# Optimization experiments

Measured on AMD Instinct MI355X. Metric: run time of the kernel, lower is better.

## Reference

```python
import jax, jax.numpy as jnp
import numpy as np

O, P, G, N, H, D = 3, 128, 64, 20000, 512, 128
TEMPERATURE = 0.1
EPS = 1e-12


def setup_inputs() -> dict:
    key = jax.random.key(0)
    k0, k1, k2, k3 = jax.random.split(key, 4)
    emb = jax.random.normal(k0, (O, N, H), dtype=jnp.float32)
    idx = jax.random.randint(k1, (O, P, G), 0, N)
    W1 = jax.random.normal(k2, (O, H, H), dtype=jnp.float32) * 0.02
    b1 = jnp.zeros((O, H), dtype=jnp.float32)
    W2 = jax.random.normal(k3, (O, H, D), dtype=jnp.float32) * 0.02
    b2 = jnp.zeros((O, D), dtype=jnp.float32)
    return {"emb": emb, "W1": W1, "b1": b1, "W2": W2, "b2": b2, "idx": idx}


def reference(emb, W1, b1, W2, b2, idx):
    # Per-omics pathway prototypes: gather gene rows then mean-pool.  [O,P,H]
    protos = jax.vmap(lambda e, i: jnp.mean(e[i], axis=1))(emb, idx)
    # Per-omics projection head: Linear -> ReLU -> (Dropout=identity in eval) -> Linear
    h = jax.nn.relu(jnp.einsum('oph,ohk->opk', protos, W1) + b1[:, None, :])
    z = jnp.einsum('opk,okd->opd', h, W2) + b2[:, None, :]          # [O,P,D]
    # Original loops p outer, ntype inner -> order (pathway, omics)
    z = jnp.transpose(z, (1, 0, 2)).reshape(P * O, D)                # [M,D], M=P*O
    z = z / (jnp.linalg.norm(z, axis=-1, keepdims=True) + EPS)       # l2 normalize
    y = jnp.repeat(jnp.arange(P), O)                                 # pathway labels [M]

    sim = (z @ z.T) / TEMPERATURE                                    # [M,M]
    M = sim.shape[0]
    eye = jnp.eye(M, dtype=bool)
    sim = jnp.where(eye, -jnp.inf, sim)
    pos_mask = (y[None, :] == y[:, None]) & ~eye
    exp_sim = jnp.exp(sim)                                           # exp(-inf)=0 on diagonal
    denom = exp_sim.sum(axis=1) + EPS
    pos_sum = jnp.sum(exp_sim * pos_mask.astype(exp_sim.dtype), axis=1) + EPS
    # every anchor has O-1 positives here, so all anchors are valid
    loss = -jnp.log(pos_sum / denom)
    return loss.mean()
```

## Files before the change

### kernel.cpp

```cpp
#include <hip/hip_runtime.h>
#include <math.h>

#define O_ 3
#define P_ 128
#define G_ 64
#define N_ 20000
#define H_ 512
#define D_ 128
#define M_ (O_*P_)
#define R_ 4

static constexpr float TEMP_INV = 10.0f;
static constexpr float EPS_ = 1e-12f;

__global__ __launch_bounds__(512) void k_proto_gemm1(const float* __restrict__ emb,
                                                     const int* __restrict__ idx,
                                                     const float* __restrict__ W1,
                                                     const float* __restrict__ b1,
                                                     float* __restrict__ hbuf) {
    const int blk = blockIdx.x;
    const int o = blk >> 5, pg = blk & 31;
    const int p0 = pg * R_;
    const int t = threadIdx.x;

    __shared__ int   sIdx[R_][G_];
    __shared__ float sPr[R_][H_];

    if (t < R_ * G_)
        sIdx[t >> 6][t & 63] = idx[(o * P_ + p0 + (t >> 6)) * G_ + (t & 63)];
    __syncthreads();

    {
        const int r = t >> 7, c4 = t & 127;
        const float* base = emb + (size_t)o * N_ * H_ + (size_t)c4 * 4;
        float4 acc = make_float4(0.f, 0.f, 0.f, 0.f);
        #pragma unroll 16
        for (int g = 0; g < G_; ++g) {
            const float4 v = *(const float4*)(base + (size_t)((unsigned)sIdx[r][g]) * H_);
            acc.x += v.x; acc.y += v.y; acc.z += v.z; acc.w += v.w;
        }
        const float s = 1.0f / (float)G_;
        ((float4*)sPr[r])[c4] = make_float4(acc.x * s, acc.y * s, acc.z * s, acc.w * s);
    }
    __syncthreads();

    const int k = t;
    const float bias = b1[o * H_ + k];
    float acc0 = bias, acc1 = bias, acc2 = bias, acc3 = bias;
    const float* w1 = W1 + (size_t)o * H_ * H_ + k;
    const float4* p0v = (const float4*)sPr[0];
    const float4* p1v = (const float4*)sPr[1];
    const float4* p2v = (const float4*)sPr[2];
    const float4* p3v = (const float4*)sPr[3];

    #pragma unroll 2
    for (int h4 = 0; h4 < H_ / 4; ++h4) {
        const float4 a0 = p0v[h4];
        const float4 a1 = p1v[h4];
        const float4 a2 = p2v[h4];
        const float4 a3 = p3v[h4];
        const float w_0 = w1[(size_t)(h4 * 4 + 0) * H_];
        const float w_1 = w1[(size_t)(h4 * 4 + 1) * H_];
        const float w_2 = w1[(size_t)(h4 * 4 + 2) * H_];
        const float w_3 = w1[(size_t)(h4 * 4 + 3) * H_];
        acc0 = fmaf(a0.x, w_0, fmaf(a0.y, w_1, fmaf(a0.z, w_2, fmaf(a0.w, w_3, acc0))));
        acc1 = fmaf(a1.x, w_0, fmaf(a1.y, w_1, fmaf(a1.z, w_2, fmaf(a1.w, w_3, acc1))));
        acc2 = fmaf(a2.x, w_0, fmaf(a2.y, w_1, fmaf(a2.z, w_2, fmaf(a2.w, w_3, acc2))));
        acc3 = fmaf(a3.x, w_0, fmaf(a3.y, w_1, fmaf(a3.z, w_2, fmaf(a3.w, w_3, acc3))));
    }
    float* hb = hbuf + (size_t)(o * P_ + p0) * H_ + k;
    hb[0 * H_] = fmaxf(acc0, 0.f);
    hb[1 * H_] = fmaxf(acc1, 0.f);
    hb[2 * H_] = fmaxf(acc2, 0.f);
    hb[3 * H_] = fmaxf(acc3, 0.f);
}

__global__ __launch_bounds__(128) void k_gemm2_norm(const float* __restrict__ hbuf,
                                                    const float* __restrict__ W2,
                                                    const float* __restrict__ b2,
                                                    float* __restrict__ z) {
    const int b = blockIdx.x;
    const int o = b >> 7, p = b & 127;
    const int d = threadIdx.x;

    __shared__ float sh[H_];
    ((float4*)sh)[d] = ((const float4*)(hbuf + (size_t)b * H_))[d];
    __syncthreads();

    const float* w2 = W2 + (size_t)o * H_ * D_ + d;
    float acc = b2[o * D_ + d];
    #pragma unroll 8
    for (int kk = 0; kk < H_; ++kk)
        acc = fmaf(sh[kk], w2[(size_t)kk * D_], acc);

    float s = acc * acc;
    #pragma unroll
    for (int off = 32; off > 0; off >>= 1) s += __shfl_down(s, off, 64);
    __shared__ float red[2];
    const int lane = d & 63, wid = d >> 6;
    if (lane == 0) red[wid] = s;
    __syncthreads();
    const float nrm = sqrtf(red[0] + red[1]);
    const float inv = 1.0f / (nrm + EPS_);
    z[(size_t)(p * O_ + o) * D_ + d] = acc * inv;
}

__global__ __launch_bounds__(128) void k_loss(const float* __restrict__ z,
                                              float* __restrict__ out) {
    const int i = blockIdx.x;
    const int t = threadIdx.x;
    __shared__ float zi[D_];
    zi[t] = z[(size_t)i * D_ + t];
    __syncthreads();
    const int pi = i / 3;
    float denom = 0.f, pos = 0.f;
    const float4* zi4 = (const float4*)zi;
    #pragma unroll
    for (int jj = 0; jj < 3; ++jj) {
        const int j = t + jj * 128;
        const float4* zj = (const float4*)(z + (size_t)j * D_);
        float dot = 0.f;
        #pragma unroll 8
        for (int q = 0; q < D_ / 4; ++q) {
            const float4 a = zi4[q];
            const float4 bb = zj[q];
            dot = fmaf(a.x, bb.x, fmaf(a.y, bb.y, fmaf(a.z, bb.z, fmaf(a.w, bb.w, dot))));
        }
        if (j != i) {
            const float e = __expf(dot * TEMP_INV);
            denom += e;
            if (j / 3 == pi) pos += e;
        }
    }
    #pragma unroll
    for (int off = 32; off > 0; off >>= 1) {
        denom += __shfl_down(denom, off, 64);
        pos   += __shfl_down(pos,   off, 64);
    }
    __shared__ float rd[2], rp[2];
    const int lane = t & 63, wid = t >> 6;
    if (lane == 0) { rd[wid] = denom; rp[wid] = pos; }
    __syncthreads();
    if (t == 0) {
        const float dn = rd[0] + rd[1] + EPS_;
        const float ps = rp[0] + rp[1] + EPS_;
        const float loss_i = logf(dn) - logf(ps);
        atomicAdd(out, loss_i * (1.0f / (float)M_));
    }
}

extern "C" void kernel_launch(void* const* d_in, const int* in_sizes, int n_in,
                              void* d_out, int out_size, void* d_ws, size_t ws_size,
                              hipStream_t stream) {
    const float* emb = (const float*)d_in[0];
    const float* W1  = (const float*)d_in[1];
    const float* b1  = (const float*)d_in[2];
    const float* W2  = (const float*)d_in[3];
    const float* b2  = (const float*)d_in[4];
    const int*   idx = (const int*)d_in[5];

    float* ws   = (float*)d_ws;
    float* hbuf = ws;
    float* zbuf = ws + 196608;

    hipMemsetAsync(d_out, 0, sizeof(float), stream);

    k_proto_gemm1<<<dim3(96),  dim3(512), 0, stream>>>(emb, idx, W1, b1, hbuf);
    k_gemm2_norm <<<dim3(M_),  dim3(128), 0, stream>>>(hbuf, W2, b2, zbuf);
    k_loss       <<<dim3(M_),  dim3(128), 0, stream>>>(zbuf, (float*)d_out);
}
```

Baseline: 253.4 us.

## Fuse second projection and normalization into gather/GEMM1 kernel; widen loss blocks

The second linear layer and L2 normalization now run inside the first kernel, with the hidden activations kept in shared memory instead of being written to and re-read from a global buffer. This removes one kernel launch and the global round trip for the hidden activations. GEMM2 now runs on only 96 blocks instead of 384, so there is less parallelism for the W2 reads. The GEMM1 unroll goes from 2 to 4, and the loss kernel uses 256 threads per block with a bounds check.

```diff
diff --git a/kernel.cpp b/kernel.cpp
--- a/kernel.cpp
+++ b/kernel.cpp
@@ -13,11 +13,13 @@
 static constexpr float TEMP_INV = 10.0f;
 static constexpr float EPS_ = 1e-12f;
 
-__global__ __launch_bounds__(512) void k_proto_gemm1(const float* __restrict__ emb,
-                                                     const int* __restrict__ idx,
-                                                     const float* __restrict__ W1,
-                                                     const float* __restrict__ b1,
-                                                     float* __restrict__ hbuf) {
+__global__ __launch_bounds__(512) void k_fused(const float* __restrict__ emb,
+                                               const int* __restrict__ idx,
+                                               const float* __restrict__ W1,
+                                               const float* __restrict__ b1,
+                                               const float* __restrict__ W2,
+                                               const float* __restrict__ b2,
+                                               float* __restrict__ z) {
     const int blk = blockIdx.x;
     const int o = blk >> 5, pg = blk & 31;
     const int p0 = pg * R_;
@@ -25,6 +27,8 @@
 
     __shared__ int   sIdx[R_][G_];
     __shared__ float sPr[R_][H_];
+    __shared__ float sH[R_][H_];
+    __shared__ float red[8];
 
     if (t < R_ * G_)
         sIdx[t >> 6][t & 63] = idx[(o * P_ + p0 + (t >> 6)) * G_ + (t & 63)];
@@ -44,92 +48,86 @@
     }
     __syncthreads();
 
-    const int k = t;
-    const float bias = b1[o * H_ + k];
-    float acc0 = bias, acc1 = bias, acc2 = bias, acc3 = bias;
-    const float* w1 = W1 + (size_t)o * H_ * H_ + k;
-    const float4* p0v = (const float4*)sPr[0];
-    const float4* p1v = (const float4*)sPr[1];
-    const float4* p2v = (const float4*)sPr[2];
-    const float4* p3v = (const float4*)sPr[3];
+    {
+        const int k = t;
+        const float bias = b1[o * H_ + k];
+        float acc0 = bias, acc1 = bias, acc2 = bias, acc3 = bias;
+        const float* w1 = W1 + (size_t)o * H_ * H_ + k;
+        const float4* p0v = (const float4*)sPr[0];
+        const float4* p1v = (const float4*)sPr[1];
+        const float4* p2v = (const float4*)sPr[2];
+        const float4* p3v = (const float4*)sPr[3];
 
-    #pragma unroll 2
-    for (int h4 = 0; h4 < H_ / 4; ++h4) {
-        const float4 a0 = p0v[h4];
-        const float4 a1 = p1v[h4];
-        const float4 a2 = p2v[h4];
-        const float4 a3 = p3v[h4];
-        const float w_0 = w1[(size_t)(h4 * 4 + 0) * H_];
-        const float w_1 = w1[(size_t)(h4 * 4 + 1) * H_];
-        const float w_2 = w1[(size_t)(h4 * 4 + 2) * H_];
-        const float w_3 = w1[(size_t)(h4 * 4 + 3) * H_];
-        acc0 = fmaf(a0.x, w_0, fmaf(a0.y, w_1, fmaf(a0.z, w_2, fmaf(a0.w, w_3, acc0))));
-        acc1 = fmaf(a1.x, w_0, fmaf(a1.y, w_1, fmaf(a1.z, w_2, fmaf(a1.w, w_3, acc1))));
-        acc2 = fmaf(a2.x, w_0, fmaf(a2.y, w_1, fmaf(a2.z, w_2, fmaf(a2.w, w_3, acc2))));
-        acc3 = fmaf(a3.x, w_0, fmaf(a3.y, w_1, fmaf(a3.z, w_2, fmaf(a3.w, w_3, acc3))));
+        #pragma unroll 4
+        for (int h4 = 0; h4 < H_ / 4; ++h4) {
+            const float4 a0 = p0v[h4];
+            const float4 a1 = p1v[h4];
+            const float4 a2 = p2v[h4];
+            const float4 a3 = p3v[h4];
+            const float w_0 = w1[(size_t)(h4 * 4 + 0) * H_];
+            const float w_1 = w1[(size_t)(h4 * 4 + 1) * H_];
+            const float w_2 = w1[(size_t)(h4 * 4 + 2) * H_];
+            const float w_3 = w1[(size_t)(h4 * 4 + 3) * H_];
+            acc0 = fmaf(a0.x, w_0, fmaf(a0.y, w_1, fmaf(a0.z, w_2, fmaf(a0.w, w_3, acc0))));
+            acc1 = fmaf(a1.x, w_0, fmaf(a1.y, w_1, fmaf(a1.z, w_2, fmaf(a1.w, w_3, acc1))));
+            acc2 = fmaf(a2.x, w_0, fmaf(a2.y, w_1, fmaf(a2.z, w_2, fmaf(a2.w, w_3, acc2))));
+            acc3 = fmaf(a3.x, w_0, fmaf(a3.y, w_1, fmaf(a3.z, w_2, fmaf(a3.w, w_3, acc3))));
+        }
+        sH[0][k] = fmaxf(acc0, 0.f);
+        sH[1][k] = fmaxf(acc1, 0.f);
+        sH[2][k] = fmaxf(acc2, 0.f);
+        sH[3][k] = fmaxf(acc3, 0.f);
     }
-    float* hb = hbuf + (size_t)(o * P_ + p0) * H_ + k;
-    hb[0 * H_] = fmaxf(acc0, 0.f);
-    hb[1 * H_] = fmaxf(acc1, 0.f);
-    hb[2 * H_] = fmaxf(acc2, 0.f);
-    hb[3 * H_] = fmaxf(acc3, 0.f);
+    __syncthreads();
+
+    {
+        const int d = t & 127, rr = t >> 7;
+        const float* hr = sH[rr];
+        const float* w2 = W2 + (size_t)o * H_ * D_ + d;
+        float acc = b2[o * D_ + d];
+        #pragma unroll 8
+        for (int kk = 0; kk < H_; ++kk)
+            acc = fmaf(hr[kk], w2[(size_t)kk * D_], acc);
+
+        float s = acc * acc;
+        #pragma unroll
+        for (int off = 32; off > 0; off >>= 1) s += __shfl_down(s, off, 64);
+        const int lane = t & 63, widg = t >> 6;
+        if (lane == 0) red[widg] = s;
+        __syncthreads();
+        const float nrm = sqrtf(red[rr * 2] + red[rr * 2 + 1]);
+        const float inv = 1.0f / (nrm + EPS_);
+        z[(size_t)((p0 + rr) * O_ + o) * D_ + d] = acc * inv;
+    }
 }
 
-__global__ __launch_bounds__(128) void k_gemm2_norm(const float* __restrict__ hbuf,
-                                                    const float* __restrict__ W2,
-                                                    const float* __restrict__ b2,
-                                                    float* __restrict__ z) {
-    const int b = blockIdx.x;
-    const int o = b >> 7, p = b & 127;
-    const int d = threadIdx.x;
-
-    __shared__ float sh[H_];
-    ((float4*)sh)[d] = ((const float4*)(hbuf + (size_t)b * H_))[d];
-    __syncthreads();
-
-    const float* w2 = W2 + (size_t)o * H_ * D_ + d;
-    float acc = b2[o * D_ + d];
-    #pragma unroll 8
-    for (int kk = 0; kk < H_; ++kk)
-        acc = fmaf(sh[kk], w2[(size_t)kk * D_], acc);
-
-    float s = acc * acc;
-    #pragma unroll
-    for (int off = 32; off > 0; off >>= 1) s += __shfl_down(s, off, 64);
-    __shared__ float red[2];
-    const int lane = d & 63, wid = d >> 6;
-    if (lane == 0) red[wid] = s;
-    __syncthreads();
-    const float nrm = sqrtf(red[0] + red[1]);
-    const float inv = 1.0f / (nrm + EPS_);
-    z[(size_t)(p * O_ + o) * D_ + d] = acc * inv;
-}
-
-__global__ __launch_bounds__(128) void k_loss(const float* __restrict__ z,
+__global__ __launch_bounds__(256) void k_loss(const float* __restrict__ z,
                                               float* __restrict__ out) {
     const int i = blockIdx.x;
     const int t = threadIdx.x;
     __shared__ float zi[D_];
-    zi[t] = z[(size_t)i * D_ + t];
+    if (t < D_) zi[t] = z[(size_t)i * D_ + t];
     __syncthreads();
     const int pi = i / 3;
     float denom = 0.f, pos = 0.f;
     const float4* zi4 = (const float4*)zi;
     #pragma unroll
-    for (int jj = 0; jj < 3; ++jj) {
-        const int j = t + jj * 128;
-        const float4* zj = (const float4*)(z + (size_t)j * D_);
-        float dot = 0.f;
-        #pragma unroll 8
-        for (int q = 0; q < D_ / 4; ++q) {
-            const float4 a = zi4[q];
-            const float4 bb = zj[q];
-            dot = fmaf(a.x, bb.x, fmaf(a.y, bb.y, fmaf(a.z, bb.z, fmaf(a.w, bb.w, dot))));
-        }
-        if (j != i) {
-            const float e = __expf(dot * TEMP_INV);
-            denom += e;
-            if (j / 3 == pi) pos += e;
+    for (int jj = 0; jj < 2; ++jj) {
+        const int j = t + jj * 256;
+        if (j < M_) {
+            const float4* zj = (const float4*)(z + (size_t)j * D_);
+            float dot = 0.f;
+            #pragma unroll 8
+            for (int q = 0; q < D_ / 4; ++q) {
+                const float4 a = zi4[q];
+                const float4 bb = zj[q];
+                dot = fmaf(a.x, bb.x, fmaf(a.y, bb.y, fmaf(a.z, bb.z, fmaf(a.w, bb.w, dot))));
+            }
+            if (j != i) {
+                const float e = __expf(dot * TEMP_INV);
+                denom += e;
+                if (j / 3 == pi) pos += e;
+            }
         }
     }
     #pragma unroll
@@ -137,13 +135,13 @@
         denom += __shfl_down(denom, off, 64);
         pos   += __shfl_down(pos,   off, 64);
     }
-    __shared__ float rd[2], rp[2];
+    __shared__ float rd[4], rp[4];
     const int lane = t & 63, wid = t >> 6;
     if (lane == 0) { rd[wid] = denom; rp[wid] = pos; }
     __syncthreads();
     if (t == 0) {
-        const float dn = rd[0] + rd[1] + EPS_;
-        const float ps = rp[0] + rp[1] + EPS_;
+        const float dn = rd[0] + rd[1] + rd[2] + rd[3] + EPS_;
+        const float ps = rp[0] + rp[1] + rp[2] + rp[3] + EPS_;
         const float loss_i = logf(dn) - logf(ps);
         atomicAdd(out, loss_i * (1.0f / (float)M_));
     }
@@ -159,13 +157,10 @@
     const float* b2  = (const float*)d_in[4];
     const int*   idx = (const int*)d_in[5];
 
-    float* ws   = (float*)d_ws;
-    float* hbuf = ws;
-    float* zbuf = ws + 196608;
+    float* zbuf = (float*)d_ws;
 
     hipMemsetAsync(d_out, 0, sizeof(float), stream);
 
-    k_proto_gemm1<<<dim3(96),  dim3(512), 0, stream>>>(emb, idx, W1, b1, hbuf);
-    k_gemm2_norm <<<dim3(M_),  dim3(128), 0, stream>>>(hbuf, W2, b2, zbuf);
-    k_loss       <<<dim3(M_),  dim3(128), 0, stream>>>(zbuf, (float*)d_out);
+    k_fused<<<dim3(96), dim3(512), 0, stream>>>(emb, idx, W1, b1, W2, b2, zbuf);
+    k_loss <<<dim3(M_), dim3(256), 0, stream>>>(zbuf, (float*)d_out);
 }
```

Result: slower. 303.1 us (+19.6%).
